# Kernel tuning notes

Hardware: AMD Instinct MI355X
Metric: run time of the kernel (lower is better)

## Reference

```python
import jax, jax.numpy as jnp
import numpy as np

N_NODES = 50000
N_EDGES = 1600000
IN_CH = 512
OUT_CH = 64
ITERATIONS = 3


def _spmm(adj_index, adj_values, x):
    # sparse @ dense: out[r] = sum_{e: row[e]==r} vals[e] * x[col[e]]
    row, col = adj_index[0], adj_index[1]
    gathered = adj_values[:, None] * x[col]  # [E, F]
    return jax.ops.segment_sum(gathered, row, num_segments=x.shape[0])


def setup_inputs() -> dict:
    key = jax.random.key(0)
    k1, k2, k3, k4, k5 = jax.random.split(key, 5)
    adj_index = jax.random.randint(k1, (2, N_EDGES), 0, N_NODES, dtype=jnp.int64)
    # positive normalized-like edge weights ~ 1/avg_degree
    adj_values = jax.random.uniform(k2, (N_EDGES,), dtype=jnp.float32) / 32.0
    features = jax.random.normal(k3, (N_NODES, IN_CH), dtype=jnp.float32)
    xavier_w = float(np.sqrt(6.0 / (IN_CH + OUT_CH)))
    weight_matrix = jax.random.uniform(k4, (IN_CH, OUT_CH), dtype=jnp.float32, minval=-xavier_w, maxval=xavier_w)
    xavier_b = float(np.sqrt(6.0 / (1 + OUT_CH)))
    bias = jax.random.uniform(k5, (1, OUT_CH), dtype=jnp.float32, minval=-xavier_b, maxval=xavier_b)
    return {"adj_index": adj_index, "adj_values": adj_values, "features": features,
            "weight_matrix": weight_matrix, "bias": bias}


def reference(adj_index, adj_values, features, weight_matrix, bias):
    # dense projection (dropout_rate=0.0 / eval mode -> identity dropout)
    base = features @ weight_matrix  # [N, OUT_CH]
    # repeated sparse-dense propagation: A^(iterations-1) @ (X W)
    for _ in range(ITERATIONS - 1):
        base = _spmm(adj_index, adj_values, base)
    return base + bias
```

## Files before the change

kernel.cpp:

```cpp
#include <hip/hip_runtime.h>
#include <hip/hip_bf16.h>

typedef __attribute__((ext_vector_type(8))) __bf16 bf16x8;
typedef __attribute__((ext_vector_type(4))) float f32x4;

#define IN_CH 512
#define OUT_CH 64
#define BS 98
#define NB 512
#define CHUNK 8192
#define CAP 4096

__device__ inline unsigned short f2bf(float f) {
    __hip_bfloat16 h = __float2bfloat16(f);
    return __builtin_bit_cast(unsigned short, h);
}
__device__ inline float bf2f(unsigned short u) {
    return __uint_as_float(((unsigned)u) << 16);
}

__global__ __launch_bounds__(512) void prep_kernel(
    const float* __restrict__ W, __hip_bfloat16* __restrict__ Wf,
    int* __restrict__ bcur)
{
    const int t = blockIdx.x * 512 + threadIdx.x;
    if (t < NB) bcur[t] = t * CAP;
    const int ct = t >> 10;
    const int rem = t & 1023;
    const int ks = rem >> 6;
    const int l = rem & 63;
    const int col = ct * 16 + (l & 15);
    const int kb = ks * 32 + (l >> 4) * 8;
    __hip_bfloat16* dst = Wf + (size_t)t * 8;
    #pragma unroll
    for (int j = 0; j < 8; ++j)
        dst[j] = (__hip_bfloat16)W[(size_t)(kb + j) * OUT_CH + col];
}

__global__ __launch_bounds__(128) void gemm_kernel(
    const float* __restrict__ A, const bf16x8* __restrict__ wf,
    __hip_bfloat16* __restrict__ outb, int N)
{
    __shared__ __align__(16) char Abf[32 * 1024];

    const int tid = threadIdx.x;
    const int row0 = blockIdx.x * 32;

    float4 v[8], vn[8];
    #pragma unroll
    for (int j = 0; j < 8; ++j) {
        int f = j * 128 + tid;
        int row = f >> 7, c4 = f & 127;
        int rg = row0 + row; rg = rg < N ? rg : N - 1;
        v[j] = *(const float4*)(A + (size_t)rg * IN_CH + c4 * 4);
    }
    #pragma unroll 1
    for (int ob = 0; ob < 4; ++ob) {
        if (ob < 3) {
            #pragma unroll
            for (int j = 0; j < 8; ++j) {
                int f = ((ob + 1) * 8 + j) * 128 + tid;
                int row = f >> 7, c4 = f & 127;
                int rg = row0 + row; rg = rg < N ? rg : N - 1;
                vn[j] = *(const float4*)(A + (size_t)rg * IN_CH + c4 * 4);
            }
        }
        #pragma unroll
        for (int j = 0; j < 8; ++j) {
            int f = (ob * 8 + j) * 128 + tid;
            int row = f >> 7, c4 = f & 127;
            int blk = c4 >> 1, half = c4 & 1;
            ushort4 h;
            h.x = f2bf(v[j].x); h.y = f2bf(v[j].y);
            h.z = f2bf(v[j].z); h.w = f2bf(v[j].w);
            *(ushort4*)(Abf + row * 1024 + ((blk ^ (row & 7)) << 4) + (half << 3)) = h;
        }
        #pragma unroll
        for (int j = 0; j < 8; ++j) v[j] = vn[j];
    }
    __syncthreads();

    const int lane = tid & 63;
    const int wave = tid >> 6;
    const int arow = wave * 16 + (lane & 15);
    const int kgb = lane >> 4;

    bf16x8 a[16];
    #pragma unroll
    for (int ks = 0; ks < 16; ++ks)
        a[ks] = *(const bf16x8*)(Abf + arow * 1024 +
                                 (((ks * 4 + kgb) ^ (arow & 7)) << 4));

    const int colb = lane & 15;
    const int rr = row0 + wave * 16 + (lane >> 4) * 4;
    #pragma unroll 1
    for (int ct = 0; ct < 4; ++ct) {
        bf16x8 w[16];
        #pragma unroll
        for (int ks = 0; ks < 16; ++ks) w[ks] = wf[(ct * 16 + ks) * 64 + lane];
        f32x4 acc = {0.f, 0.f, 0.f, 0.f};
        #pragma unroll
        for (int ks = 0; ks < 16; ++ks)
            acc = __builtin_amdgcn_mfma_f32_16x16x32_bf16(a[ks], w[ks], acc, 0, 0, 0);
        int col = ct * 16 + colb;
        #pragma unroll
        for (int i = 0; i < 4; ++i) {
            int r = rr + i;
            if (r < N)
                outb[(size_t)r * OUT_CH + col] = __float2bfloat16(acc[i]);
        }
    }
}

__global__ __launch_bounds__(512) void bucket_scatter_kernel(
    const int* __restrict__ rows, const int* __restrict__ cols,
    const float* __restrict__ vals, int* __restrict__ bcur,
    unsigned* __restrict__ segc, unsigned char* __restrict__ segr, int E)
{
    __shared__ unsigned      c_lds[CHUNK];
    __shared__ unsigned char r_lds[CHUNK];
    __shared__ unsigned short b_lds[CHUNK];
    __shared__ int hist[NB];
    __shared__ int scn[NB];
    __shared__ int lbase[NB];
    __shared__ int runBase[NB];

    const int tid = threadIdx.x;
    const int c0 = blockIdx.x * CHUNK;
    const int cnt = min(CHUNK, E - c0);
    const int base = c0 + tid * 16;

    hist[tid] = 0;
    __syncthreads();

    int myb[16]; unsigned myc[16]; unsigned char myr[16];
    int nmine = 0;
    if (base + 16 <= E) {
        nmine = 16;
        int4 r4[4], c4[4]; float4 v4[4];
        #pragma unroll
        for (int q = 0; q < 4; ++q) {
            r4[q] = *(const int4*)(rows + base + q * 4);
            c4[q] = *(const int4*)(cols + base + q * 4);
            v4[q] = *(const float4*)(vals + base + q * 4);
        }
        #pragma unroll
        for (int q = 0; q < 4; ++q) {
            int rr[4] = {r4[q].x, r4[q].y, r4[q].z, r4[q].w};
            int cc[4] = {c4[q].x, c4[q].y, c4[q].z, c4[q].w};
            float vv[4] = {v4[q].x, v4[q].y, v4[q].z, v4[q].w};
            #pragma unroll
            for (int u = 0; u < 4; ++u) {
                int j = q * 4 + u;
                int r = rr[u];
                int b = r / BS;
                myb[j] = b;
                myr[j] = (unsigned char)(r - b * BS);
                myc[j] = ((unsigned)cc[u] << 16) | f2bf(vv[u]);
                atomicAdd(&hist[b], 1);
            }
        }
    } else {
        #pragma unroll 1
        for (int j = 0; j < 16; ++j) {
            int e = base + j;
            if (e < E) {
                int r = rows[e];
                int b = r / BS;
                myb[j] = b;
                myr[j] = (unsigned char)(r - b * BS);
                myc[j] = ((unsigned)cols[e] << 16) | f2bf(vals[e]);
                atomicAdd(&hist[b], 1);
                nmine = j + 1;
            }
        }
    }
    __syncthreads();

    {
        int h = hist[tid];
        scn[tid] = h;
        __syncthreads();
        for (int ofs = 1; ofs < NB; ofs <<= 1) {
            int u = 0;
            if (tid >= ofs) u = scn[tid - ofs];
            __syncthreads();
            if (tid >= ofs) scn[tid] += u;
            __syncthreads();
        }
        int excl = scn[tid] - h;
        lbase[tid] = excl;
        hist[tid] = excl;
        runBase[tid] = h ? atomicAdd(&bcur[tid], h) : 0;
    }
    __syncthreads();

    #pragma unroll 1
    for (int j = 0; j < nmine; ++j) {
        int pos = atomicAdd(&hist[myb[j]], 1);
        c_lds[pos] = myc[j];
        r_lds[pos] = myr[j];
        b_lds[pos] = (unsigned short)myb[j];
    }
    __syncthreads();

    for (int idx = tid; idx < cnt; idx += 512) {
        int b = b_lds[idx];
        int gpos = runBase[b] + (idx - lbase[b]);
        segc[gpos] = c_lds[idx];
        segr[gpos] = r_lds[idx];
    }
}

__global__ __launch_bounds__(512) void sortspmm_kernel(
    const int* __restrict__ bcur,
    unsigned* __restrict__ segc, const unsigned char* __restrict__ segr,
    int* __restrict__ offs, int* __restrict__ rend,
    const __hip_bfloat16* __restrict__ x,
    __hip_bfloat16* __restrict__ y1, int N)
{
    __shared__ unsigned sorted4[CAP];
    __shared__ int hist[BS + 1];
    __shared__ int cursor[BS];

    const int b = blockIdx.x;
    const int t = threadIdx.x;
    const int s = b * CAP;
    const int cnt = bcur[b] - s;

    if (t < BS + 1) hist[t] = 0;
    __syncthreads();

    unsigned ek[8]; unsigned char er[8];
    #pragma unroll
    for (int j = 0; j < 8; ++j) {
        int idx = t + j * 512;
        if (idx < cnt) {
            ek[j] = segc[s + idx];
            er[j] = segr[s + idx];
            atomicAdd(&hist[er[j]], 1);
        }
    }
    __syncthreads();

    if (t == 0) {
        int run = 0;
        for (int i = 0; i < BS; ++i) { int c = hist[i]; hist[i] = run; run += c; }
        hist[BS] = run;
    }
    __syncthreads();

    if (t < BS) {
        cursor[t] = hist[t];
        offs[b * BS + t] = s + hist[t];
        rend[b * BS + t] = s + hist[t + 1];
    }
    __syncthreads();

    #pragma unroll
    for (int j = 0; j < 8; ++j) {
        int idx = t + j * 512;
        if (idx < cnt) {
            int pos = atomicAdd(&cursor[er[j]], 1);
            sorted4[pos] = ek[j];
        }
    }
    __syncthreads();

    #pragma unroll
    for (int j = 0; j < 8; ++j) {
        int idx = t + j * 512;
        if (idx < cnt) segc[s + idx] = sorted4[idx];
    }

    const int lane = t & 63;
    const int wave = t >> 6;
    const int grp = lane >> 4;
    const int l16 = lane & 15;
    const ushort* xp = (const ushort*)x + l16 * 4;

    #pragma unroll 1
    for (int sweep = 0; sweep < 4; ++sweep) {
        int rr = sweep * 32 + wave * 4 + grp;
        int rrc = rr < BS ? rr : BS - 1;
        int rs = hist[rrc];
        int re = hist[rrc + 1];
        int gr = b * BS + rr;
        if (rr >= BS || gr >= N) re = rs;

        float4 acc = {0.f, 0.f, 0.f, 0.f};
        for (int i0 = rs; i0 < re; i0 += 16) {
            unsigned p[16];
            #pragma unroll
            for (int j = 0; j < 16; ++j) {
                int idx = i0 + j;
                p[j] = sorted4[idx < re ? idx : rs];
            }
            ushort4 xv[16];
            #pragma unroll
            for (int j = 0; j < 16; ++j)
                xv[j] = *(const ushort4*)(xp + (size_t)(p[j] >> 16) * OUT_CH);
            #pragma unroll
            for (int j = 0; j < 16; ++j) {
                float wv = (i0 + j < re) ? __uint_as_float(p[j] << 16) : 0.f;
                acc.x = fmaf(wv, bf2f(xv[j].x), acc.x);
                acc.y = fmaf(wv, bf2f(xv[j].y), acc.y);
                acc.z = fmaf(wv, bf2f(xv[j].z), acc.z);
                acc.w = fmaf(wv, bf2f(xv[j].w), acc.w);
            }
        }
        if (rr < BS && gr < N) {
            ushort4 h;
            h.x = f2bf(acc.x); h.y = f2bf(acc.y);
            h.z = f2bf(acc.z); h.w = f2bf(acc.w);
            *(ushort4*)((ushort*)y1 + (size_t)gr * OUT_CH + l16 * 4) = h;
        }
    }
}

__global__ __launch_bounds__(256) void spmm_row_kernel(
    const int* __restrict__ offs, const int* __restrict__ rend,
    const unsigned* __restrict__ segc,
    const __hip_bfloat16* __restrict__ x,
    float* __restrict__ yf, const float* __restrict__ bias, int N)
{
    const int tid = threadIdx.x;
    const int lane = tid & 63;
    const int wave = tid >> 6;
    const int grp = lane >> 4;
    const int l16 = lane & 15;

    int r = (blockIdx.x * 4 + wave) * 4 + grp;
    const bool rv = r < N;
    const int rc = rv ? r : N - 1;
    const int s = offs[rc];
    const int e = rv ? rend[rc] : s;

    int m = e - s;
    m = max(m, __shfl_xor(m, 16));
    m = max(m, __shfl_xor(m, 32));
    const int iters = (m + 15) >> 4;

    const ushort* xp = (const ushort*)x + l16 * 4;

    float4 acc = {0.f, 0.f, 0.f, 0.f};
    for (int it = 0; it < iters; ++it) {
        const int base = s + it * 16;
        unsigned p[16];
        #pragma unroll
        for (int j = 0; j < 16; ++j) {
            int idx = base + j;
            p[j] = segc[idx < e ? idx : s];
        }
        ushort4 xv[16];
        #pragma unroll
        for (int j = 0; j < 16; ++j)
            xv[j] = *(const ushort4*)(xp + (size_t)(p[j] >> 16) * OUT_CH);
        #pragma unroll
        for (int j = 0; j < 16; ++j) {
            int idx = base + j;
            float wv = (idx < e) ? __uint_as_float(p[j] << 16) : 0.f;
            acc.x = fmaf(wv, bf2f(xv[j].x), acc.x);
            acc.y = fmaf(wv, bf2f(xv[j].y), acc.y);
            acc.z = fmaf(wv, bf2f(xv[j].z), acc.z);
            acc.w = fmaf(wv, bf2f(xv[j].w), acc.w);
        }
    }

    if (rv) {
        float4 bv = *(const float4*)(bias + l16 * 4);
        float4 o;
        o.x = acc.x + bv.x; o.y = acc.y + bv.y;
        o.z = acc.z + bv.z; o.w = acc.w + bv.w;
        *(float4*)(yf + (size_t)r * OUT_CH + l16 * 4) = o;
    }
}

static inline size_t align_up(size_t v) { return (v + 255) & ~(size_t)255; }

extern "C" void kernel_launch(void* const* d_in, const int* in_sizes, int n_in,
                              void* d_out, int out_size, void* d_ws, size_t ws_size,
                              hipStream_t stream)
{
    const int*   adj  = (const int*)d_in[0];
    const float* vals = (const float*)d_in[1];
    const float* feat = (const float*)d_in[2];
    const float* Wm   = (const float*)d_in[3];
    const float* bias = (const float*)d_in[4];

    const int E = in_sizes[1];
    const int N = in_sizes[2] / IN_CH;
    const int* rows  = adj;
    const int* colsI = adj + E;

    char* w = (char*)d_ws;
    size_t o = 0;
    __hip_bfloat16* B0b = (__hip_bfloat16*)(w + o); o += align_up((size_t)N * OUT_CH * 2);
    __hip_bfloat16* Y1b = (__hip_bfloat16*)(w + o); o += align_up((size_t)N * OUT_CH * 2);
    __hip_bfloat16* Wf  = (__hip_bfloat16*)(w + o); o += align_up((size_t)IN_CH * OUT_CH * 2);
    int*           bcur = (int*)          (w + o); o += align_up(NB * sizeof(int));
    int*           offs = (int*)          (w + o); o += align_up((size_t)NB * BS * sizeof(int));
    int*           rend = (int*)          (w + o); o += align_up((size_t)NB * BS * sizeof(int));
    unsigned*      segc = (unsigned*)     (w + o); o += align_up((size_t)NB * CAP * sizeof(unsigned));
    unsigned char* segr = (unsigned char*)(w + o); o += align_up((size_t)NB * CAP);
    (void)ws_size; (void)n_in; (void)out_size;

    prep_kernel<<<8, 512, 0, stream>>>(Wm, Wf, bcur);

    gemm_kernel<<<(N + 31) / 32, 128, 0, stream>>>(
        feat, (const bf16x8*)Wf, B0b, N);

    bucket_scatter_kernel<<<(E + CHUNK - 1) / CHUNK, 512, 0, stream>>>(
        rows, colsI, vals, bcur, segc, segr, E);

    sortspmm_kernel<<<NB, 512, 0, stream>>>(
        bcur, segc, segr, offs, rend, B0b, Y1b, N);

    spmm_row_kernel<<<(N + 15) / 16, 256, 0, stream>>>(
        offs, rend, segc, Y1b, (float*)d_out, bias, N);
}
```

Measured before the change: 113.4 us.

## Fuse GEMM and bucket scatter into one heterogeneous kernel launch

```diff
diff --git a/kernel.cpp b/kernel.cpp
--- a/kernel.cpp
+++ b/kernel.cpp
@@ -8,7 +8,7 @@
 #define OUT_CH 64
 #define BS 98
 #define NB 512
-#define CHUNK 8192
+#define CHUNK 4096
 #define CAP 4096
 
 __device__ inline unsigned short f2bf(float f) {
@@ -37,37 +37,125 @@
         dst[j] = (__hip_bfloat16)W[(size_t)(kb + j) * OUT_CH + col];
 }
 
-__global__ __launch_bounds__(128) void gemm_kernel(
+__global__ __launch_bounds__(512, 4) void gemmscatter_kernel(
+    const int* __restrict__ rows, const int* __restrict__ cols,
+    const float* __restrict__ vals, int* __restrict__ bcur,
+    unsigned* __restrict__ segc, unsigned char* __restrict__ segr, int E,
+    int nScatter,
     const float* __restrict__ A, const bf16x8* __restrict__ wf,
     __hip_bfloat16* __restrict__ outb, int N)
 {
-    __shared__ __align__(16) char Abf[32 * 1024];
-
+    __shared__ __align__(16) char smem[36 * 1024];
     const int tid = threadIdx.x;
-    const int row0 = blockIdx.x * 32;
-
-    float4 v[8], vn[8];
-    #pragma unroll
-    for (int j = 0; j < 8; ++j) {
-        int f = j * 128 + tid;
-        int row = f >> 7, c4 = f & 127;
-        int rg = row0 + row; rg = rg < N ? rg : N - 1;
-        v[j] = *(const float4*)(A + (size_t)rg * IN_CH + c4 * 4);
-    }
-    #pragma unroll 1
-    for (int ob = 0; ob < 4; ++ob) {
-        if (ob < 3) {
+
+    if (blockIdx.x < nScatter) {
+        unsigned*       c_lds = (unsigned*)smem;
+        unsigned char*  r_lds = (unsigned char*)(smem + 16384);
+        unsigned short* b_lds = (unsigned short*)(smem + 20480);
+        int* hist    = (int*)(smem + 28672);
+        int* scn     = (int*)(smem + 30720);
+        int* lbase   = (int*)(smem + 32768);
+        int* runBase = (int*)(smem + 34816);
+
+        const int c0 = blockIdx.x * CHUNK;
+        const int cnt = min(CHUNK, E - c0);
+        const int base = c0 + tid * 8;
+
+        hist[tid] = 0;
+        __syncthreads();
+
+        int myb[8]; unsigned myc[8]; unsigned char myr[8];
+        int nmine = 0;
+        if (base + 8 <= E) {
+            nmine = 8;
+            int4 r4[2], c4[2]; float4 v4[2];
             #pragma unroll
+            for (int q = 0; q < 2; ++q) {
+                r4[q] = *(const int4*)(rows + base + q * 4);
+                c4[q] = *(const int4*)(cols + base + q * 4);
+                v4[q] = *(const float4*)(vals + base + q * 4);
+            }
+            #pragma unroll
+            for (int q = 0; q < 2; ++q) {
+                int rr[4] = {r4[q].x, r4[q].y, r4[q].z, r4[q].w};
+                int cc[4] = {c4[q].x, c4[q].y, c4[q].z, c4[q].w};
+                float vv[4] = {v4[q].x, v4[q].y, v4[q].z, v4[q].w};
+                #pragma unroll
+                for (int u = 0; u < 4; ++u) {
+                    int j = q * 4 + u;
+                    int r = rr[u];
+                    int b = r / BS;
+                    myb[j] = b;
+                    myr[j] = (unsigned char)(r - b * BS);
+                    myc[j] = ((unsigned)cc[u] << 16) | f2bf(vv[u]);
+                    atomicAdd(&hist[b], 1);
+                }
+            }
+        } else {
+            #pragma unroll 1
             for (int j = 0; j < 8; ++j) {
-                int f = ((ob + 1) * 8 + j) * 128 + tid;
-                int row = f >> 7, c4 = f & 127;
-                int rg = row0 + row; rg = rg < N ? rg : N - 1;
-                vn[j] = *(const float4*)(A + (size_t)rg * IN_CH + c4 * 4);
-            }
-        }
+                int e = base + j;
+                if (e < E) {
+                    int r = rows[e];
+                    int b = r / BS;
+                    myb[j] = b;
+                    myr[j] = (unsigned char)(r - b * BS);
+                    myc[j] = ((unsigned)cols[e] << 16) | f2bf(vals[e]);
+                    atomicAdd(&hist[b], 1);
+                    nmine = j + 1;
+                }
+            }
+        }
+        __syncthreads();
+
+        {
+            int h = hist[tid];
+            scn[tid] = h;
+            __syncthreads();
+            for (int ofs = 1; ofs < NB; ofs <<= 1) {
+                int u = 0;
+                if (tid >= ofs) u = scn[tid - ofs];
+                __syncthreads();
+                if (tid >= ofs) scn[tid] += u;
+                __syncthreads();
+            }
+            int excl = scn[tid] - h;
+            lbase[tid] = excl;
+            hist[tid] = excl;
+            runBase[tid] = h ? atomicAdd(&bcur[tid], h) : 0;
+        }
+        __syncthreads();
+
+        #pragma unroll 1
+        for (int j = 0; j < nmine; ++j) {
+            int pos = atomicAdd(&hist[myb[j]], 1);
+            c_lds[pos] = myc[j];
+            r_lds[pos] = myr[j];
+            b_lds[pos] = (unsigned short)myb[j];
+        }
+        __syncthreads();
+
+        for (int idx = tid; idx < cnt; idx += 512) {
+            int b = b_lds[idx];
+            int gpos = runBase[b] + (idx - lbase[b]);
+            segc[gpos] = c_lds[idx];
+            segr[gpos] = r_lds[idx];
+        }
+    } else {
+        char* Abf = smem;
+        const int row0 = (blockIdx.x - nScatter) * 32;
+
+        float4 v[8];
         #pragma unroll
         for (int j = 0; j < 8; ++j) {
-            int f = (ob * 8 + j) * 128 + tid;
+            int f = j * 512 + tid;
+            int row = f >> 7, c4 = f & 127;
+            int rg = row0 + row; rg = rg < N ? rg : N - 1;
+            v[j] = *(const float4*)(A + (size_t)rg * IN_CH + c4 * 4);
+        }
+        #pragma unroll
+        for (int j = 0; j < 8; ++j) {
+            int f = j * 512 + tid;
             int row = f >> 7, c4 = f & 127;
             int blk = c4 >> 1, half = c4 & 1;
             ushort4 h;
@@ -75,140 +163,35 @@
             h.z = f2bf(v[j].z); h.w = f2bf(v[j].w);
             *(ushort4*)(Abf + row * 1024 + ((blk ^ (row & 7)) << 4) + (half << 3)) = h;
         }
-        #pragma unroll
-        for (int j = 0; j < 8; ++j) v[j] = vn[j];
-    }
-    __syncthreads();
-
-    const int lane = tid & 63;
-    const int wave = tid >> 6;
-    const int arow = wave * 16 + (lane & 15);
-    const int kgb = lane >> 4;
-
-    bf16x8 a[16];
-    #pragma unroll
-    for (int ks = 0; ks < 16; ++ks)
-        a[ks] = *(const bf16x8*)(Abf + arow * 1024 +
-                                 (((ks * 4 + kgb) ^ (arow & 7)) << 4));
-
-    const int colb = lane & 15;
-    const int rr = row0 + wave * 16 + (lane >> 4) * 4;
-    #pragma unroll 1
-    for (int ct = 0; ct < 4; ++ct) {
-        bf16x8 w[16];
-        #pragma unroll
-        for (int ks = 0; ks < 16; ++ks) w[ks] = wf[(ct * 16 + ks) * 64 + lane];
+        __syncthreads();
+
+        const int lane = tid & 63;
+        const int wave = tid >> 6;
+        const int rowblk = wave & 1;
+        const int ct = wave >> 1;
+        const int arow = rowblk * 16 + (lane & 15);
+        const int kgb = lane >> 4;
+
+        bf16x8 a[16];
+        #pragma unroll
+        for (int ks = 0; ks < 16; ++ks)
+            a[ks] = *(const bf16x8*)(Abf + arow * 1024 +
+                                     (((ks * 4 + kgb) ^ (arow & 7)) << 4));
+
         f32x4 acc = {0.f, 0.f, 0.f, 0.f};
         #pragma unroll
         for (int ks = 0; ks < 16; ++ks)
-            acc = __builtin_amdgcn_mfma_f32_16x16x32_bf16(a[ks], w[ks], acc, 0, 0, 0);
-        int col = ct * 16 + colb;
+            acc = __builtin_amdgcn_mfma_f32_16x16x32_bf16(
+                a[ks], wf[(ct * 16 + ks) * 64 + lane], acc, 0, 0, 0);
+
+        const int col = ct * 16 + (lane & 15);
+        const int rr = row0 + rowblk * 16 + (lane >> 4) * 4;
         #pragma unroll
         for (int i = 0; i < 4; ++i) {
             int r = rr + i;
             if (r < N)
                 outb[(size_t)r * OUT_CH + col] = __float2bfloat16(acc[i]);
         }
-    }
-}
-
-__global__ __launch_bounds__(512) void bucket_scatter_kernel(
-    const int* __restrict__ rows, const int* __restrict__ cols,
-    const float* __restrict__ vals, int* __restrict__ bcur,
-    unsigned* __restrict__ segc, unsigned char* __restrict__ segr, int E)
-{
-    __shared__ unsigned      c_lds[CHUNK];
-    __shared__ unsigned char r_lds[CHUNK];
-    __shared__ unsigned short b_lds[CHUNK];
-    __shared__ int hist[NB];
-    __shared__ int scn[NB];
-    __shared__ int lbase[NB];
-    __shared__ int runBase[NB];
-
-    const int tid = threadIdx.x;
-    const int c0 = blockIdx.x * CHUNK;
-    const int cnt = min(CHUNK, E - c0);
-    const int base = c0 + tid * 16;
-
-    hist[tid] = 0;
-    __syncthreads();
-
-    int myb[16]; unsigned myc[16]; unsigned char myr[16];
-    int nmine = 0;
-    if (base + 16 <= E) {
-        nmine = 16;
-        int4 r4[4], c4[4]; float4 v4[4];
-        #pragma unroll
-        for (int q = 0; q < 4; ++q) {
-            r4[q] = *(const int4*)(rows + base + q * 4);
-            c4[q] = *(const int4*)(cols + base + q * 4);
-            v4[q] = *(const float4*)(vals + base + q * 4);
-        }
-        #pragma unroll
-        for (int q = 0; q < 4; ++q) {
-            int rr[4] = {r4[q].x, r4[q].y, r4[q].z, r4[q].w};
-            int cc[4] = {c4[q].x, c4[q].y, c4[q].z, c4[q].w};
-            float vv[4] = {v4[q].x, v4[q].y, v4[q].z, v4[q].w};
-            #pragma unroll
-            for (int u = 0; u < 4; ++u) {
-                int j = q * 4 + u;
-                int r = rr[u];
-                int b = r / BS;
-                myb[j] = b;
-                myr[j] = (unsigned char)(r - b * BS);
-                myc[j] = ((unsigned)cc[u] << 16) | f2bf(vv[u]);
-                atomicAdd(&hist[b], 1);
-            }
-        }
-    } else {
-        #pragma unroll 1
-        for (int j = 0; j < 16; ++j) {
-            int e = base + j;
-            if (e < E) {
-                int r = rows[e];
-                int b = r / BS;
-                myb[j] = b;
-                myr[j] = (unsigned char)(r - b * BS);
-                myc[j] = ((unsigned)cols[e] << 16) | f2bf(vals[e]);
-                atomicAdd(&hist[b], 1);
-                nmine = j + 1;
-            }
-        }
-    }
-    __syncthreads();
-
-    {
-        int h = hist[tid];
-        scn[tid] = h;
-        __syncthreads();
-        for (int ofs = 1; ofs < NB; ofs <<= 1) {
-            int u = 0;
-            if (tid >= ofs) u = scn[tid - ofs];
-            __syncthreads();
-            if (tid >= ofs) scn[tid] += u;
-            __syncthreads();
-        }
-        int excl = scn[tid] - h;
-        lbase[tid] = excl;
-        hist[tid] = excl;
-        runBase[tid] = h ? atomicAdd(&bcur[tid], h) : 0;
-    }
-    __syncthreads();
-
-    #pragma unroll 1
-    for (int j = 0; j < nmine; ++j) {
-        int pos = atomicAdd(&hist[myb[j]], 1);
-        c_lds[pos] = myc[j];
-        r_lds[pos] = myr[j];
-        b_lds[pos] = (unsigned short)myb[j];
-    }
-    __syncthreads();
-
-    for (int idx = tid; idx < cnt; idx += 512) {
-        int b = b_lds[idx];
-        int gpos = runBase[b] + (idx - lbase[b]);
-        segc[gpos] = c_lds[idx];
-        segr[gpos] = r_lds[idx];
     }
 }
 
@@ -407,11 +390,11 @@
 
     prep_kernel<<<8, 512, 0, stream>>>(Wm, Wf, bcur);
 
-    gemm_kernel<<<(N + 31) / 32, 128, 0, stream>>>(
+    const int nScatter = (E + CHUNK - 1) / CHUNK;
+    const int nGemm = (N + 31) / 32;
+    gemmscatter_kernel<<<nScatter + nGemm, 512, 0, stream>>>(
+        rows, colsI, vals, bcur, segc, segr, E, nScatter,
         feat, (const bf16x8*)Wf, B0b, N);
-
-    bucket_scatter_kernel<<<(E + CHUNK - 1) / CHUNK, 512, 0, stream>>>(
-        rows, colsI, vals, bcur, segc, segr, E);
 
     sortspmm_kernel<<<NB, 512, 0, stream>>>(
         bcur, segc, segr, offs, rend, B0b, Y1b, N);
```

After: 101.1 us, median of 2. -10.9%, faster.
